# Performance work log

Hardware: AMD Instinct MI355X
Metric: run time of the kernel (lower is better)

## Reference

```python
import jax, jax.numpy as jnp
import numpy as np

B, L, H, Z = 16, 2048, 1024, 512
NEG = -1e9


def setup_inputs() -> dict:
    key = jax.random.key(0)
    ks = jax.random.split(key, 7)
    return {
        "encoder_rnn_hidden_states": jax.random.normal(ks[0], (B, L, H), jnp.float32),
        "encoder_final_hidden_state": jax.random.normal(ks[1], (B, H), jnp.float32),
        "latent_z_seq": jax.random.normal(ks[2], (B, L, Z), jnp.float32),
        "mask": jax.random.randint(ks[3], (B, L), 0, 2, jnp.int32),
        "weight_q": jax.random.normal(ks[4], (H, H), jnp.float32),
        "weight_k": jax.random.normal(ks[5], (H, H), jnp.float32),
        "weight_v": jax.random.normal(ks[6], (Z, Z), jnp.float32),
    }


def reference(encoder_rnn_hidden_states, encoder_final_hidden_state, latent_z_seq,
              mask, weight_q, weight_k, weight_v):
    temperature = jnp.asarray(weight_q.shape[0] ** 0.5, encoder_rnn_hidden_states.dtype)
    # final hidden state is repeated along src_len, so project once: [B,H]
    k = encoder_final_hidden_state @ weight_k              # [B,H]
    q = encoder_rnn_hidden_states @ weight_q               # [B,L,H]
    v = latent_z_seq @ weight_v                            # [B,L,Z]
    # alignment[b,i,j] = q[b,i] . k[b]  (identical across j, per original repeat)
    alignment = jnp.einsum('bih,bh->bi', q, k) / temperature  # [B,L]
    alignment = jnp.broadcast_to(alignment[:, :, None], (q.shape[0], q.shape[1], q.shape[1]))
    # mask[:, :, None] tiled over last dim; fill -1e9 where mask == 0
    alignment = jnp.where(mask[:, :, None] == 0, NEG, alignment)
    # softmax over the QUERY axis (dim=-2), not the usual key axis
    attn = jax.nn.softmax(alignment, axis=-2)              # [B,L,L]
    output = jnp.einsum('bij,bjz->biz', attn, v)           # [B,L,Z]
    return output, attn
```

## Files before the change

### kernel.cpp

```cpp
#include <hip/hip_runtime.h>

#define BB 16
#define LL 2048
#define HH 1024
#define ZZ 512
#define NEGV -1e9f

__global__ void k_proj_k(const float* __restrict__ efhs,
                         const float* __restrict__ Wk,
                         float* __restrict__ kout) {
    int idx = blockIdx.x * 256 + threadIdx.x;
    int b = idx >> 10, hp = idx & 1023;
    const float* e = efhs + b * HH;
    float acc = 0.f;
    for (int h = 0; h < HH; ++h)
        acc += e[h] * Wk[h * HH + hp];
    kout[idx] = acc;
}

__global__ void k_proj_kq(const float* __restrict__ Wq,
                          const float* __restrict__ kin,
                          float* __restrict__ kq) {
    int row = blockIdx.x * 4 + (threadIdx.x >> 6);
    int lane = threadIdx.x & 63;
    int b = row >> 10, h = row & 1023;
    const float4* wrow = (const float4*)(Wq + (size_t)h * HH);
    const float4* kb = (const float4*)(kin + b * HH);
    float acc = 0.f;
#pragma unroll
    for (int u = 0; u < 4; ++u) {
        float4 wv = wrow[u * 64 + lane];
        float4 kv = kb[u * 64 + lane];
        acc += wv.x * kv.x + wv.y * kv.y + wv.z * kv.z + wv.w * kv.w;
    }
    for (int off = 32; off > 0; off >>= 1) acc += __shfl_down(acc, off);
    if (lane == 0) kq[row] = acc;
}

__global__ void k_zsum(const float* __restrict__ zseq,
                       float* __restrict__ zsum) {
    int b = blockIdx.x >> 5;
    int jc = blockIdx.x & 31;
    int z0 = threadIdx.x;
    const float* p = zseq + ((size_t)(b * LL + jc * 64)) * ZZ + z0;
    float acc = 0.f;
    for (int j = 0; j < 64; ++j) acc += p[(size_t)j * ZZ];
    atomicAdd(&zsum[b * ZZ + z0], acc);
}

__global__ void k_vsum(const float* __restrict__ zsum,
                       const float* __restrict__ Wv,
                       float* __restrict__ Vs) {
    int idx = blockIdx.x * 256 + threadIdx.x;
    int b = idx >> 9, z = idx & 511;
    const float* zs = zsum + b * ZZ;
    float acc = 0.f;
    for (int z0 = 0; z0 < ZZ; ++z0) acc += zs[z0] * Wv[z0 * ZZ + z];
    Vs[idx] = acc;
}

__global__ void k_scores(const float* __restrict__ erhs,
                         const float* __restrict__ kq,
                         const int* __restrict__ mask,
                         float* __restrict__ s) {
    int row = blockIdx.x * 4 + (threadIdx.x >> 6);
    int lane = threadIdx.x & 63;
    int b = row >> 11;
    const float4* e = (const float4*)(erhs + (size_t)row * HH);
    const float4* kb = (const float4*)(kq + b * HH);
    float acc = 0.f;
#pragma unroll
    for (int u = 0; u < 4; ++u) {
        float4 ev = e[u * 64 + lane];
        float4 kv = kb[u * 64 + lane];
        acc += ev.x * kv.x + ev.y * kv.y + ev.z * kv.z + ev.w * kv.w;
    }
    for (int off = 32; off > 0; off >>= 1) acc += __shfl_down(acc, off);
    if (lane == 0) {
        float v = acc * (1.0f / 32.0f);
        if (mask[row] == 0) v = NEGV;
        s[row] = v;
    }
}

__global__ void k_softmax(const float* __restrict__ s, float* __restrict__ w) {
    __shared__ float es[LL];
    __shared__ float red[16];
    int b = blockIdx.x, tid = threadIdx.x;
    int wave = tid >> 6, lane = tid & 63;
    const float* sb = s + b * LL;
    float m = -3.4e38f;
    for (int i = tid; i < LL; i += 256) m = fmaxf(m, sb[i]);
    for (int off = 32; off > 0; off >>= 1) m = fmaxf(m, __shfl_down(m, off));
    if (lane == 0) red[wave] = m;
    __syncthreads();
    if (tid == 0) {
        float mm = red[0];
        for (int i = 1; i < 4; ++i) mm = fmaxf(mm, red[i]);
        red[0] = mm;
    }
    __syncthreads();
    m = red[0];
    float ssum = 0.f;
    for (int i = tid; i < LL; i += 256) {
        float e = __expf(sb[i] - m);
        es[i] = e;
        ssum += e;
    }
    for (int off = 32; off > 0; off >>= 1) ssum += __shfl_down(ssum, off);
    if (lane == 0) red[8 + wave] = ssum;
    __syncthreads();
    if (tid == 0) {
        float t = 0.f;
        for (int i = 0; i < 4; ++i) t += red[8 + i];
        red[8] = t;
    }
    __syncthreads();
    float inv = 1.0f / red[8];
    for (int i = tid; i < LL; i += 256) w[b * LL + i] = es[i] * inv;
}

__global__ void k_out(const float* __restrict__ w, const float* __restrict__ Vs,
                      float* __restrict__ out) {
    int idx = blockIdx.x * 256 + threadIdx.x;
    int b = idx >> 18;
    int rem = idx & 262143;
    int i = rem >> 7, zv = rem & 127;
    float wv = w[b * LL + i];
    float4 v = ((const float4*)(Vs + b * ZZ))[zv];
    ((float4*)out)[idx] = make_float4(wv * v.x, wv * v.y, wv * v.z, wv * v.w);
}

__global__ void k_attn(const float* __restrict__ w, float* __restrict__ attn) {
    int row = blockIdx.x;
    float v = w[row];
    float4 pk = make_float4(v, v, v, v);
    float4* p = (float4*)attn + (size_t)row * 512;
    p[threadIdx.x] = pk;
    p[threadIdx.x + 256] = pk;
}

extern "C" void kernel_launch(void* const* d_in, const int* in_sizes, int n_in,
                              void* d_out, int out_size, void* d_ws, size_t ws_size,
                              hipStream_t stream) {
    const float* erhs = (const float*)d_in[0];
    const float* efhs = (const float*)d_in[1];
    const float* zseq = (const float*)d_in[2];
    const int*   mask = (const int*)d_in[3];
    const float* Wq   = (const float*)d_in[4];
    const float* Wk   = (const float*)d_in[5];
    const float* Wv   = (const float*)d_in[6];
    float* out = (float*)d_out;

    float* ws   = (float*)d_ws;
    float* zsum = ws;
    float* kbuf = ws + 8192;
    float* kq   = ws + 24576;
    float* Vs   = ws + 40960;
    float* sbuf = ws + 49152;
    float* wbuf = ws + 81920;

    hipMemsetAsync(zsum, 0, 8192 * sizeof(float), stream);
    k_proj_k <<<   64, 256, 0, stream>>>(efhs, Wk, kbuf);
    k_proj_kq<<< 4096, 256, 0, stream>>>(Wq, kbuf, kq);
    k_zsum   <<<  512, 512, 0, stream>>>(zseq, zsum);
    k_vsum   <<<   32, 256, 0, stream>>>(zsum, Wv, Vs);
    k_scores <<< 8192, 256, 0, stream>>>(erhs, kq, mask, sbuf);
    k_softmax<<<   16, 256, 0, stream>>>(sbuf, wbuf);
    k_out    <<<16384, 256, 0, stream>>>(wbuf, Vs, out);
    k_attn   <<<32768, 256, 0, stream>>>(wbuf, out + (size_t)BB * LL * ZZ);
}
```

Measured before the change: 551.8 us.

## Fuse independent stages into shared launches and split small matvecs across blocks

Merges zsum into the scores launch, the V-projection into the softmax launch, and the output and attn writes into one launch, cutting eight kernel launches to five. k_proj_k and the V-projection are split along the reduction dimension over many more blocks and combined with atomics, so these serial matvecs no longer run on only a few dozen blocks. k_proj_kq is reordered so one block handles one Wq row for four batches, letting that row be reused. The cost is atomic accumulation, which changes summation order, plus a larger memset.

```diff
diff --git a/kernel.cpp b/kernel.cpp
--- a/kernel.cpp
+++ b/kernel.cpp
@@ -6,26 +6,31 @@
 #define ZZ 512
 #define NEGV -1e9f
 
-__global__ void k_proj_k(const float* __restrict__ efhs,
-                         const float* __restrict__ Wk,
-                         float* __restrict__ kout) {
-    int idx = blockIdx.x * 256 + threadIdx.x;
-    int b = idx >> 10, hp = idx & 1023;
-    const float* e = efhs + b * HH;
+__global__ __launch_bounds__(256) void k_proj_k(const float* __restrict__ efhs,
+                                                const float* __restrict__ Wk,
+                                                float* __restrict__ kbuf) {
+    int blk = blockIdx.x;
+    int b   = blk >> 5;
+    int hpc = (blk >> 3) & 3;
+    int hc  = blk & 7;
+    int hp  = hpc * 256 + threadIdx.x;
+    const float* e  = efhs + b * HH + hc * 128;
+    const float* wk = Wk + (size_t)(hc * 128) * HH + hp;
     float acc = 0.f;
-    for (int h = 0; h < HH; ++h)
-        acc += e[h] * Wk[h * HH + hp];
-    kout[idx] = acc;
+#pragma unroll 4
+    for (int h = 0; h < 128; ++h)
+        acc += e[h] * wk[(size_t)h * HH];
+    atomicAdd(&kbuf[b * HH + hp], acc);
 }
 
-__global__ void k_proj_kq(const float* __restrict__ Wq,
-                          const float* __restrict__ kin,
-                          float* __restrict__ kq) {
-    int row = blockIdx.x * 4 + (threadIdx.x >> 6);
+__global__ __launch_bounds__(256) void k_proj_kq(const float* __restrict__ Wq,
+                                                 const float* __restrict__ kbuf,
+                                                 float* __restrict__ kq) {
+    int h = blockIdx.x >> 2;
+    int b = ((blockIdx.x & 3) << 2) + (threadIdx.x >> 6);
     int lane = threadIdx.x & 63;
-    int b = row >> 10, h = row & 1023;
     const float4* wrow = (const float4*)(Wq + (size_t)h * HH);
-    const float4* kb = (const float4*)(kin + b * HH);
+    const float4* kb   = (const float4*)(kbuf + b * HH);
     float acc = 0.f;
 #pragma unroll
     for (int u = 0; u < 4; ++u) {
@@ -34,110 +39,125 @@
         acc += wv.x * kv.x + wv.y * kv.y + wv.z * kv.z + wv.w * kv.w;
     }
     for (int off = 32; off > 0; off >>= 1) acc += __shfl_down(acc, off);
-    if (lane == 0) kq[row] = acc;
+    if (lane == 0) kq[b * HH + h] = acc;
 }
 
-__global__ void k_zsum(const float* __restrict__ zseq,
-                       float* __restrict__ zsum) {
-    int b = blockIdx.x >> 5;
-    int jc = blockIdx.x & 31;
-    int z0 = threadIdx.x;
-    const float* p = zseq + ((size_t)(b * LL + jc * 64)) * ZZ + z0;
-    float acc = 0.f;
-    for (int j = 0; j < 64; ++j) acc += p[(size_t)j * ZZ];
-    atomicAdd(&zsum[b * ZZ + z0], acc);
-}
-
-__global__ void k_vsum(const float* __restrict__ zsum,
-                       const float* __restrict__ Wv,
-                       float* __restrict__ Vs) {
-    int idx = blockIdx.x * 256 + threadIdx.x;
-    int b = idx >> 9, z = idx & 511;
-    const float* zs = zsum + b * ZZ;
-    float acc = 0.f;
-    for (int z0 = 0; z0 < ZZ; ++z0) acc += zs[z0] * Wv[z0 * ZZ + z];
-    Vs[idx] = acc;
-}
-
-__global__ void k_scores(const float* __restrict__ erhs,
-                         const float* __restrict__ kq,
-                         const int* __restrict__ mask,
-                         float* __restrict__ s) {
-    int row = blockIdx.x * 4 + (threadIdx.x >> 6);
-    int lane = threadIdx.x & 63;
-    int b = row >> 11;
-    const float4* e = (const float4*)(erhs + (size_t)row * HH);
-    const float4* kb = (const float4*)(kq + b * HH);
-    float acc = 0.f;
+__global__ __launch_bounds__(256) void k_scores_zsum(const float* __restrict__ erhs,
+                                                     const float* __restrict__ kq,
+                                                     const int* __restrict__ mask,
+                                                     const float* __restrict__ zseq,
+                                                     float* __restrict__ sbuf,
+                                                     float* __restrict__ zsum) {
+    if (blockIdx.x < 8192) {
+        int row = blockIdx.x * 4 + (threadIdx.x >> 6);
+        int lane = threadIdx.x & 63;
+        int b = row >> 11;
+        const float4* e  = (const float4*)(erhs + (size_t)row * HH);
+        const float4* kb = (const float4*)(kq + b * HH);
+        float acc = 0.f;
 #pragma unroll
-    for (int u = 0; u < 4; ++u) {
-        float4 ev = e[u * 64 + lane];
-        float4 kv = kb[u * 64 + lane];
-        acc += ev.x * kv.x + ev.y * kv.y + ev.z * kv.z + ev.w * kv.w;
-    }
-    for (int off = 32; off > 0; off >>= 1) acc += __shfl_down(acc, off);
-    if (lane == 0) {
-        float v = acc * (1.0f / 32.0f);
-        if (mask[row] == 0) v = NEGV;
-        s[row] = v;
+        for (int u = 0; u < 4; ++u) {
+            float4 ev = e[u * 64 + lane];
+            float4 kv = kb[u * 64 + lane];
+            acc += ev.x * kv.x + ev.y * kv.y + ev.z * kv.z + ev.w * kv.w;
+        }
+        for (int off = 32; off > 0; off >>= 1) acc += __shfl_down(acc, off);
+        if (lane == 0) {
+            float v = acc * (1.0f / 32.0f);
+            if (mask[row] == 0) v = NEGV;
+            sbuf[row] = v;
+        }
+    } else {
+        int blk = blockIdx.x - 8192;
+        int b = blk >> 5, jc = blk & 31;
+        int t = threadIdx.x;
+        const float* p = zseq + ((size_t)(b * LL + jc * 64)) * ZZ;
+        float a0 = 0.f, a1 = 0.f;
+        for (int j = 0; j < 64; ++j) {
+            const float* pj = p + (size_t)j * ZZ;
+            a0 += pj[t];
+            a1 += pj[t + 256];
+        }
+        atomicAdd(&zsum[b * ZZ + t], a0);
+        atomicAdd(&zsum[b * ZZ + t + 256], a1);
     }
 }
 
-__global__ void k_softmax(const float* __restrict__ s, float* __restrict__ w) {
+__global__ __launch_bounds__(256) void k_softmax_vsum(const float* __restrict__ sbuf,
+                                                      const float* __restrict__ zsum,
+                                                      const float* __restrict__ Wv,
+                                                      float* __restrict__ wbuf,
+                                                      float* __restrict__ Vs) {
     __shared__ float es[LL];
     __shared__ float red[16];
-    int b = blockIdx.x, tid = threadIdx.x;
-    int wave = tid >> 6, lane = tid & 63;
-    const float* sb = s + b * LL;
-    float m = -3.4e38f;
-    for (int i = tid; i < LL; i += 256) m = fmaxf(m, sb[i]);
-    for (int off = 32; off > 0; off >>= 1) m = fmaxf(m, __shfl_down(m, off));
-    if (lane == 0) red[wave] = m;
-    __syncthreads();
-    if (tid == 0) {
-        float mm = red[0];
-        for (int i = 1; i < 4; ++i) mm = fmaxf(mm, red[i]);
-        red[0] = mm;
+    if (blockIdx.x < 16) {
+        int b = blockIdx.x, tid = threadIdx.x;
+        int wave = tid >> 6, lane = tid & 63;
+        const float* sb = sbuf + b * LL;
+        float m = -3.4e38f;
+        for (int i = tid; i < LL; i += 256) m = fmaxf(m, sb[i]);
+        for (int off = 32; off > 0; off >>= 1) m = fmaxf(m, __shfl_down(m, off));
+        if (lane == 0) red[wave] = m;
+        __syncthreads();
+        if (tid == 0) {
+            float mm = red[0];
+            for (int i = 1; i < 4; ++i) mm = fmaxf(mm, red[i]);
+            red[0] = mm;
+        }
+        __syncthreads();
+        m = red[0];
+        float ssum = 0.f;
+        for (int i = tid; i < LL; i += 256) {
+            float e = __expf(sb[i] - m);
+            es[i] = e;
+            ssum += e;
+        }
+        for (int off = 32; off > 0; off >>= 1) ssum += __shfl_down(ssum, off);
+        if (lane == 0) red[8 + wave] = ssum;
+        __syncthreads();
+        if (tid == 0) {
+            float tt = 0.f;
+            for (int i = 0; i < 4; ++i) tt += red[8 + i];
+            red[8] = tt;
+        }
+        __syncthreads();
+        float inv = 1.0f / red[8];
+        for (int i = tid; i < LL; i += 256) wbuf[b * LL + i] = es[i] * inv;
+    } else {
+        int blk = blockIdx.x - 16;
+        int b = blk >> 3, z0c = blk & 7;
+        int t = threadIdx.x;
+        const float* zs = zsum + b * ZZ + z0c * 64;
+        const float* wv = Wv + (size_t)(z0c * 64) * ZZ;
+        float a0 = 0.f, a1 = 0.f;
+        for (int z0 = 0; z0 < 64; ++z0) {
+            float zv = zs[z0];
+            const float* wr = wv + (size_t)z0 * ZZ;
+            a0 += zv * wr[t];
+            a1 += zv * wr[t + 256];
+        }
+        atomicAdd(&Vs[b * ZZ + t], a0);
+        atomicAdd(&Vs[b * ZZ + t + 256], a1);
     }
-    __syncthreads();
-    m = red[0];
-    float ssum = 0.f;
-    for (int i = tid; i < LL; i += 256) {
-        float e = __expf(sb[i] - m);
-        es[i] = e;
-        ssum += e;
-    }
-    for (int off = 32; off > 0; off >>= 1) ssum += __shfl_down(ssum, off);
-    if (lane == 0) red[8 + wave] = ssum;
-    __syncthreads();
-    if (tid == 0) {
-        float t = 0.f;
-        for (int i = 0; i < 4; ++i) t += red[8 + i];
-        red[8] = t;
-    }
-    __syncthreads();
-    float inv = 1.0f / red[8];
-    for (int i = tid; i < LL; i += 256) w[b * LL + i] = es[i] * inv;
 }
 
-__global__ void k_out(const float* __restrict__ w, const float* __restrict__ Vs,
-                      float* __restrict__ out) {
-    int idx = blockIdx.x * 256 + threadIdx.x;
-    int b = idx >> 18;
-    int rem = idx & 262143;
-    int i = rem >> 7, zv = rem & 127;
-    float wv = w[b * LL + i];
-    float4 v = ((const float4*)(Vs + b * ZZ))[zv];
-    ((float4*)out)[idx] = make_float4(wv * v.x, wv * v.y, wv * v.z, wv * v.w);
-}
-
-__global__ void k_attn(const float* __restrict__ w, float* __restrict__ attn) {
+__global__ __launch_bounds__(256) void k_outattn(const float* __restrict__ wbuf,
+                                                 const float* __restrict__ Vs,
+                                                 float* __restrict__ out,
+                                                 float* __restrict__ attn) {
     int row = blockIdx.x;
-    float v = w[row];
-    float4 pk = make_float4(v, v, v, v);
+    int b = row >> 11;
+    int t = threadIdx.x;
+    float wv = wbuf[row];
+    if (t < 128) {
+        float4 v = ((const float4*)(Vs + b * ZZ))[t];
+        ((float4*)(out + (size_t)row * ZZ))[t] =
+            make_float4(wv * v.x, wv * v.y, wv * v.z, wv * v.w);
+    }
+    float4 pk = make_float4(wv, wv, wv, wv);
     float4* p = (float4*)attn + (size_t)row * 512;
-    p[threadIdx.x] = pk;
-    p[threadIdx.x + 256] = pk;
+    p[t]       = pk;
+    p[t + 256] = pk;
 }
 
 extern "C" void kernel_launch(void* const* d_in, const int* in_sizes, int n_in,
@@ -155,18 +175,16 @@
     float* ws   = (float*)d_ws;
     float* zsum = ws;
     float* kbuf = ws + 8192;
-    float* kq   = ws + 24576;
-    float* Vs   = ws + 40960;
-    float* sbuf = ws + 49152;
-    float* wbuf = ws + 81920;
+    float* Vs   = ws + 24576;
+    float* sbuf = ws + 32768;
+    float* wbuf = ws + 65536;
+    float* kq   = ws + 98304;
 
-    hipMemsetAsync(zsum, 0, 8192 * sizeof(float), stream);
-    k_proj_k <<<   64, 256, 0, stream>>>(efhs, Wk, kbuf);
-    k_proj_kq<<< 4096, 256, 0, stream>>>(Wq, kbuf, kq);
-    k_zsum   <<<  512, 512, 0, stream>>>(zseq, zsum);
-    k_vsum   <<<   32, 256, 0, stream>>>(zsum, Wv, Vs);
-    k_scores <<< 8192, 256, 0, stream>>>(erhs, kq, mask, sbuf);
-    k_softmax<<<   16, 256, 0, stream>>>(sbuf, wbuf);
-    k_out    <<<16384, 256, 0, stream>>>(wbuf, Vs, out);
-    k_attn   <<<32768, 256, 0, stream>>>(wbuf, out + (size_t)BB * LL * ZZ);
+    hipMemsetAsync(ws, 0, 32768 * sizeof(float), stream);
+    k_proj_k      <<<  512, 256, 0, stream>>>(efhs, Wk, kbuf);
+    k_proj_kq     <<< 4096, 256, 0, stream>>>(Wq, kbuf, kq);
+    k_scores_zsum <<< 8704, 256, 0, stream>>>(erhs, kq, mask, zseq, sbuf, zsum);
+    k_softmax_vsum<<<  144, 256, 0, stream>>>(sbuf, zsum, Wv, wbuf, Vs);
+    k_outattn     <<<32768, 256, 0, stream>>>(wbuf, Vs, out,
+                                              out + (size_t)BB * LL * ZZ);
 }
```

Measured after the change: 503.4 us. 1.1x faster.
